# Performance work log

Hardware: AMD Instinct MI355X
Metric: run time of the kernel (lower is better)

The kernel has to match this reference:

```python
import jax, jax.numpy as jnp
import numpy as np

WS = 11      # window_size
SIGMA = 1.5
C1 = 0.01 ** 2
C2 = 0.03 ** 2


def _window(channel):
    g = np.exp(-((np.arange(WS) - WS // 2) ** 2) / (2.0 * SIGMA ** 2))
    g = (g / g.sum()).astype(np.float32)
    w2 = np.outer(g, g)  # [WS, WS]
    return jnp.asarray(np.broadcast_to(w2, (channel, 1, WS, WS)).copy())


def _blur(x, w, channel):
    pad = WS // 2
    return jax.lax.conv_general_dilated(
        x, w, window_strides=(1, 1), padding=[(pad, pad), (pad, pad)],
        dimension_numbers=("NCHW", "OIHW", "NCHW"),
        feature_group_count=channel)


def _ssim(img1, img2, w, channel):
    mu1 = _blur(img1, w, channel)
    mu2 = _blur(img2, w, channel)
    mu1_sq = mu1 * mu1
    mu2_sq = mu2 * mu2
    mu1_mu2 = mu1 * mu2
    sigma1_sq = _blur(img1 * img1, w, channel) - mu1_sq
    sigma2_sq = _blur(img2 * img2, w, channel) - mu2_sq
    sigma12 = _blur(img1 * img2, w, channel) - mu1_mu2
    ssim_map = ((2.0 * mu1_mu2 + C1) * (2.0 * sigma12 + C2)) / (
        (mu1_sq + mu2_sq + C1) * (sigma1_sq + sigma2_sq + C2))
    return ssim_map.mean()  # size_average=True


def setup_inputs() -> dict:
    key = jax.random.key(0)
    k1, k2, k3 = jax.random.split(key, 3)
    B, C, H, W = 16, 3, 512, 512
    return {
        "fused_img": jax.random.uniform(k1, (B, C, H, W), dtype=jnp.float32),
        "source_img1": jax.random.uniform(k2, (B, C, H, W), dtype=jnp.float32),
        "source_img2": jax.random.uniform(k3, (B, C, H, W), dtype=jnp.float32),
    }


def reference(fused_img, source_img1, source_img2):
    channel = fused_img.shape[1]
    w = _window(channel).astype(fused_img.dtype)
    ssim1 = _ssim(fused_img, source_img1, w, channel)
    ssim2 = _ssim(fused_img, source_img2, w, channel)
    return 1.0 - (ssim1 + ssim2) / 2.0
```

## Files before the change

### kernel.cpp

```cpp
#include <hip/hip_runtime.h>
#include <cmath>

#define HALO 5
#define TSX 32
#define TILE_H 128
#define NSTEP 8
#define CH 16
#define RING 42
#define HSTR 36
#define PLANE (RING * HSTR)
#define WIDTH 512
#define HEIGHT 512

struct GW { float g[11]; };

__device__ __forceinline__ float ssim2(float mu1, float mu2,
                                       float x2b, float y2b, float xyb)
{
    const float C1 = 1e-4f, C2 = 9e-4f;
    float mu12 = mu1 * mu2;
    float num  = (2.f * mu12 + C1) * (2.f * (xyb - mu12) + C2);
    float den  = (mu1 * mu1 + mu2 * mu2 + C1) *
                 ((x2b - mu1 * mu1) + (y2b - mu2 * mu2) + C2);
    return num * __builtin_amdgcn_rcpf(den);
}

template<bool CX, bool CY>
__device__ __forceinline__ void hblur_row(
    const float* __restrict__ rowf, const float* __restrict__ rowa,
    const float* __restrict__ rowb, bool yok, int gx0, int slot, int qA,
    float (* __restrict__ hb)[PLANE], const GW& gw)
{
    float acc[4][8];
    #pragma unroll
    for (int jj = 0; jj < 4; ++jj)
        #pragma unroll
        for (int q = 0; q < 8; ++q) acc[jj][q] = 0.f;

    #pragma unroll
    for (int k = 0; k < 5; ++k) {
        const int g = gx0 + 4 * k;
        float4 vf, va, vb;
        if (CX || CY) {
            bool ok = true;
            if (CY) ok = yok;
            if (CX) ok = ok && ((unsigned)g <= (unsigned)(WIDTH - 4));
            vf = ok ? *(const float4*)(rowf + g) : make_float4(0,0,0,0);
            va = ok ? *(const float4*)(rowa + g) : make_float4(0,0,0,0);
            vb = ok ? *(const float4*)(rowb + g) : make_float4(0,0,0,0);
        } else {
            vf = *(const float4*)(rowf + g);
            va = *(const float4*)(rowa + g);
            vb = *(const float4*)(rowb + g);
        }
        const float fs[4] = { vf.x, vf.y, vf.z, vf.w };
        const float as[4] = { va.x, va.y, va.z, va.w };
        const float bs[4] = { vb.x, vb.y, vb.z, vb.w };
        #pragma unroll
        for (int cc = 0; cc < 4; ++cc) {
            const int tt = 4 * k + cc - 3;
            if (tt < 0 || tt > 13) continue;
            const float f = fs[cc], a = as[cc], b = bs[cc];
            float p[8];
            p[0] = f; p[1] = a; p[2] = b;
            p[3] = f * f; p[4] = a * a; p[5] = b * b;
            p[6] = f * a; p[7] = f * b;
            #pragma unroll
            for (int jj = 0; jj < 4; ++jj) {
                const int u = tt - jj;
                if (u >= 0 && u <= 10) {
                    const float w = gw.g[u];
                    #pragma unroll
                    for (int q = 0; q < 8; ++q)
                        acc[jj][q] = fmaf(w, p[q], acc[jj][q]);
                }
            }
        }
    }
    #pragma unroll
    for (int q = 0; q < 8; ++q)
        *(float4*)(&hb[q][slot * HSTR + 4 * qA]) =
            make_float4(acc[0][q], acc[1][q], acc[2][q], acc[3][q]);
}

template<bool CX, bool CY>
__device__ __forceinline__ float tile_compute(
    const float* __restrict__ fI, const float* __restrict__ aI,
    const float* __restrict__ bI, float (* __restrict__ hb)[PLANE],
    const GW& gw, int tid, int x0, int y0, size_t pbase)
{
    const int rA  = tid >> 3;
    const int qA  = tid & 7;
    const int gx0 = x0 + 4 * qA - 8;
    const int jB  = tid & 31;
    const int rgB = (tid >> 5) & 3;

    float part = 0.f;

    if (rA < 26) {
        const int yy = y0 - HALO + rA;
        const bool yok = CY ? ((unsigned)yy < (unsigned)HEIGHT) : true;
        hblur_row<CX, CY>(fI + pbase + (size_t)yy * WIDTH,
                          aI + pbase + (size_t)yy * WIDTH,
                          bI + pbase + (size_t)yy * WIDTH,
                          yok, gx0, rA, qA, hb, gw);
    }
    __syncthreads();

    #pragma unroll 1
    for (int s = 0; s < NSTEP; ++s) {
        if (tid < 128) {
            if (s < NSTEP - 1) {
                const int t = CH * s + RING - CH + rA;
                int slot = t;
                slot -= (slot >= RING) ? RING : 0;
                slot -= (slot >= RING) ? RING : 0;
                slot -= (slot >= RING) ? RING : 0;
                const int yy = y0 - HALO + t;
                const bool yok = CY ? ((unsigned)yy < (unsigned)HEIGHT) : true;
                hblur_row<CX, CY>(fI + pbase + (size_t)yy * WIDTH,
                                  aI + pbase + (size_t)yy * WIDTH,
                                  bI + pbase + (size_t)yy * WIDTH,
                                  yok, gx0, slot, qA, hb, gw);
            }
        } else {
            int sb = CH * s + 4 * rgB;
            sb -= (sb >= RING) ? RING : 0;
            sb -= (sb >= RING) ? RING : 0;
            float acc2[4][8];
            #pragma unroll
            for (int ri = 0; ri < 4; ++ri)
                #pragma unroll
                for (int q = 0; q < 8; ++q) acc2[ri][q] = 0.f;
            #pragma unroll
            for (int k = 0; k < 14; ++k) {
                int t = sb + k;
                t -= (t >= RING) ? RING : 0;
                const float* hp = &hb[0][t * HSTR + jB];
                float hv[8];
                #pragma unroll
                for (int q = 0; q < 8; ++q) hv[q] = hp[q * PLANE];
                #pragma unroll
                for (int ri = 0; ri < 4; ++ri) {
                    const int u = k - ri;
                    if (u >= 0 && u <= 10) {
                        const float w = gw.g[u];
                        #pragma unroll
                        for (int q = 0; q < 8; ++q)
                            acc2[ri][q] = fmaf(w, hv[q], acc2[ri][q]);
                    }
                }
            }
            #pragma unroll
            for (int ri = 0; ri < 4; ++ri) {
                part += ssim2(acc2[ri][0], acc2[ri][1],
                              acc2[ri][3], acc2[ri][4], acc2[ri][6]);
                part += ssim2(acc2[ri][0], acc2[ri][2],
                              acc2[ri][3], acc2[ri][5], acc2[ri][7]);
            }
        }
        __syncthreads();
    }
    return part;
}

__global__ __launch_bounds__(256, 3)
void ssim_tile(const float* __restrict__ fI, const float* __restrict__ aI,
               const float* __restrict__ bI, float* __restrict__ bsum,
               GW gw)
{
    __shared__ __align__(16) float hb[8][PLANE];
    __shared__ float red[4];

    const int tid = threadIdx.x;
    const int x0 = blockIdx.x * TSX;
    const int y0 = blockIdx.y * TILE_H;
    const size_t pbase = (size_t)blockIdx.z * (size_t)(WIDTH * HEIGHT);

    const bool ex = (blockIdx.x == 0) || (blockIdx.x == gridDim.x - 1);
    const bool ey = (blockIdx.y == 0) || (blockIdx.y == gridDim.y - 1);

    float part;
    if (!ex && !ey)
        part = tile_compute<false, false>(fI, aI, bI, hb, gw, tid, x0, y0, pbase);
    else if (!ex)
        part = tile_compute<false, true >(fI, aI, bI, hb, gw, tid, x0, y0, pbase);
    else if (!ey)
        part = tile_compute<true,  false>(fI, aI, bI, hb, gw, tid, x0, y0, pbase);
    else
        part = tile_compute<true,  true >(fI, aI, bI, hb, gw, tid, x0, y0, pbase);

    #pragma unroll
    for (int off = 32; off > 0; off >>= 1) part += __shfl_down(part, off);
    if ((tid & 63) == 0) red[tid >> 6] = part;
    __syncthreads();
    if (tid == 0) {
        int bid = blockIdx.x + gridDim.x * (blockIdx.y + gridDim.y * blockIdx.z);
        bsum[bid] = red[0] + red[1] + red[2] + red[3];
    }
}

__global__ __launch_bounds__(256)
void ssim_final(const float* __restrict__ bsum, float* __restrict__ out,
                int nb, float invTwoN)
{
    __shared__ float sred[4];
    float s = 0.f;
    for (int i = threadIdx.x; i < nb; i += 256) s += bsum[i];
    #pragma unroll
    for (int off = 32; off > 0; off >>= 1) s += __shfl_down(s, off);
    if ((threadIdx.x & 63) == 0) sred[threadIdx.x >> 6] = s;
    __syncthreads();
    if (threadIdx.x == 0)
        out[0] = 1.f - (sred[0] + sred[1] + sred[2] + sred[3]) * invTwoN;
}

extern "C" void kernel_launch(void* const* d_in, const int* in_sizes, int n_in,
                              void* d_out, int out_size, void* d_ws, size_t ws_size,
                              hipStream_t stream)
{
    const float* f  = (const float*)d_in[0];
    const float* s1 = (const float*)d_in[1];
    const float* s2 = (const float*)d_in[2];
    float* out  = (float*)d_out;
    float* bsum = (float*)d_ws;

    const int N = in_sizes[0];
    const int planes = N / (WIDTH * HEIGHT);

    GW gw;
    double gd[11], gs = 0.0;
    for (int i = 0; i < 11; ++i) {
        double d = (double)(i - 5);
        gd[i] = exp(-(d * d) / 4.5);
        gs += gd[i];
    }
    for (int i = 0; i < 11; ++i) gw.g[i] = (float)(gd[i] / gs);

    dim3 grid(WIDTH / TSX, HEIGHT / TILE_H, planes);
    const int nb = (WIDTH / TSX) * (HEIGHT / TILE_H) * planes;
    ssim_tile<<<grid, dim3(256), 0, stream>>>(f, s1, s2, bsum, gw);
    ssim_final<<<1, dim3(256), 0, stream>>>(bsum, out, nb, 0.5f / (float)N);
}
```

Measured before the change: 255.9 us.

## Store horizontal blur intermediates as packed fp16 and do vertical blur in half2

The horizontal blur results are packed into fp16 pairs in shared memory, halving LDS footprint and traffic, and the vertical pass accumulates with packed half2 FMAs. This allows raising launch bounds to 6 blocks per CU for more occupancy. The cost is precision: sigma terms computed as blur(x^2)-mu^2 in fp16 suffer catastrophic cancellation, which may break the accuracy tolerance.

```diff
diff --git a/kernel.cpp b/kernel.cpp
--- a/kernel.cpp
+++ b/kernel.cpp
@@ -1,4 +1,5 @@
 #include <hip/hip_runtime.h>
+#include <hip/hip_fp16.h>
 #include <cmath>
 
 #define HALO 5
@@ -14,6 +15,12 @@
 
 struct GW { float g[11]; };
 
+__device__ __forceinline__ uint32_t pk2(float a, float b)
+{
+    auto h = __builtin_amdgcn_cvt_pkrtz(a, b);
+    return __builtin_bit_cast(uint32_t, h);
+}
+
 __device__ __forceinline__ float ssim2(float mu1, float mu2,
                                        float x2b, float y2b, float xyb)
 {
@@ -29,7 +36,7 @@
 __device__ __forceinline__ void hblur_row(
     const float* __restrict__ rowf, const float* __restrict__ rowa,
     const float* __restrict__ rowb, bool yok, int gx0, int slot, int qA,
-    float (* __restrict__ hb)[PLANE], const GW& gw)
+    uint32_t (* __restrict__ hb)[PLANE], const GW& gw)
 {
     float acc[4][8];
     #pragma unroll
@@ -78,15 +85,19 @@
         }
     }
     #pragma unroll
-    for (int q = 0; q < 8; ++q)
-        *(float4*)(&hb[q][slot * HSTR + 4 * qA]) =
-            make_float4(acc[0][q], acc[1][q], acc[2][q], acc[3][q]);
+    for (int p = 0; p < 4; ++p) {
+        uint4 v = make_uint4(pk2(acc[0][2*p], acc[0][2*p+1]),
+                             pk2(acc[1][2*p], acc[1][2*p+1]),
+                             pk2(acc[2][2*p], acc[2][2*p+1]),
+                             pk2(acc[3][2*p], acc[3][2*p+1]));
+        *(uint4*)(&hb[p][slot * HSTR + 4 * qA]) = v;
+    }
 }
 
 template<bool CX, bool CY>
 __device__ __forceinline__ float tile_compute(
     const float* __restrict__ fI, const float* __restrict__ aI,
-    const float* __restrict__ bI, float (* __restrict__ hb)[PLANE],
+    const float* __restrict__ bI, uint32_t (* __restrict__ hb)[PLANE],
     const GW& gw, int tid, int x0, int y0, size_t pbase)
 {
     const int rA  = tid >> 3;
@@ -94,6 +105,10 @@
     const int gx0 = x0 + 4 * qA - 8;
     const int jB  = tid & 31;
     const int rgB = (tid >> 5) & 3;
+
+    __half2 wh[11];
+    #pragma unroll
+    for (int i = 0; i < 11; ++i) wh[i] = __float2half2_rn(gw.g[i]);
 
     float part = 0.f;
 
@@ -127,36 +142,43 @@
             int sb = CH * s + 4 * rgB;
             sb -= (sb >= RING) ? RING : 0;
             sb -= (sb >= RING) ? RING : 0;
-            float acc2[4][8];
+            __half2 acc2[4][4];
             #pragma unroll
             for (int ri = 0; ri < 4; ++ri)
                 #pragma unroll
-                for (int q = 0; q < 8; ++q) acc2[ri][q] = 0.f;
+                for (int p = 0; p < 4; ++p)
+                    acc2[ri][p] = __float2half2_rn(0.f);
             #pragma unroll
             for (int k = 0; k < 14; ++k) {
                 int t = sb + k;
                 t -= (t >= RING) ? RING : 0;
-                const float* hp = &hb[0][t * HSTR + jB];
-                float hv[8];
+                const uint32_t* hp = &hb[0][t * HSTR + jB];
+                __half2 hv[4];
                 #pragma unroll
-                for (int q = 0; q < 8; ++q) hv[q] = hp[q * PLANE];
+                for (int p = 0; p < 4; ++p)
+                    hv[p] = __builtin_bit_cast(__half2, hp[p * PLANE]);
                 #pragma unroll
                 for (int ri = 0; ri < 4; ++ri) {
                     const int u = k - ri;
                     if (u >= 0 && u <= 10) {
-                        const float w = gw.g[u];
                         #pragma unroll
-                        for (int q = 0; q < 8; ++q)
-                            acc2[ri][q] = fmaf(w, hv[q], acc2[ri][q]);
+                        for (int p = 0; p < 4; ++p)
+                            acc2[ri][p] = __hfma2(wh[u], hv[p], acc2[ri][p]);
                     }
                 }
             }
             #pragma unroll
             for (int ri = 0; ri < 4; ++ri) {
-                part += ssim2(acc2[ri][0], acc2[ri][1],
-                              acc2[ri][3], acc2[ri][4], acc2[ri][6]);
-                part += ssim2(acc2[ri][0], acc2[ri][2],
-                              acc2[ri][3], acc2[ri][5], acc2[ri][7]);
+                const float F  = __low2float (acc2[ri][0]);
+                const float A  = __high2float(acc2[ri][0]);
+                const float B  = __low2float (acc2[ri][1]);
+                const float F2 = __high2float(acc2[ri][1]);
+                const float A2 = __low2float (acc2[ri][2]);
+                const float B2 = __high2float(acc2[ri][2]);
+                const float FA = __low2float (acc2[ri][3]);
+                const float FB = __high2float(acc2[ri][3]);
+                part += ssim2(F, A, F2, A2, FA);
+                part += ssim2(F, B, F2, B2, FB);
             }
         }
         __syncthreads();
@@ -164,12 +186,12 @@
     return part;
 }
 
-__global__ __launch_bounds__(256, 3)
+__global__ __launch_bounds__(256, 6)
 void ssim_tile(const float* __restrict__ fI, const float* __restrict__ aI,
                const float* __restrict__ bI, float* __restrict__ bsum,
                GW gw)
 {
-    __shared__ __align__(16) float hb[8][PLANE];
+    __shared__ __align__(16) uint32_t hb[4][PLANE];
     __shared__ float red[4];
 
     const int tid = threadIdx.x;
```

Measured after the change: 363.9 us. 42.2% more time.
